# Performance work log

Hardware: AMD Instinct MI355X
Metric: run time of the kernel (lower is better)

Reference implementation:

```python
import jax, jax.numpy as jnp
import numpy as np

L = 2      # layer_num
H = 64     # hid_dim == in_dim (required by final .view(B, N, F))


def setup_inputs() -> dict:
    key = jax.random.key(0)
    k = jax.random.split(key, 5)
    B, T, N, Fd = 64, 48, 256, H
    s = 1.0 / np.sqrt(H)  # PyTorch GRUCell init scale
    return {
        "x": jax.random.normal(k[0], (B, T, N, Fd), dtype=jnp.float32),
        "Wih": jax.random.uniform(k[1], (L, 3 * H, H), minval=-s, maxval=s, dtype=jnp.float32),
        "Whh": jax.random.uniform(k[2], (L, 3 * H, H), minval=-s, maxval=s, dtype=jnp.float32),
        "bih": jax.random.uniform(k[3], (L, 3 * H), minval=-s, maxval=s, dtype=jnp.float32),
        "bhh": jax.random.uniform(k[4], (L, 3 * H), minval=-s, maxval=s, dtype=jnp.float32),
    }


def _ngru_forward(x, Wih, Whh, bih, bhh):
    B, T, N, Fd = x.shape
    # (T, B*N, F): time-major sequence; each layer sees the SAME input x_t
    # (layers are parallel, not stacked, per the original module).
    xs = x.transpose(1, 0, 2, 3).reshape(T, B * N, Fd)
    h0 = jnp.zeros((L, B * N, H), dtype=x.dtype)

    def step(h, x_t):
        # gi: (L, B*N, 3H), gh: (L, B*N, 3H)
        gi = jnp.einsum('bf,lgf->lbg', x_t, Wih) + bih[:, None, :]
        gh = jnp.einsum('lbh,lgh->lbg', h, Whh) + bhh[:, None, :]
        gi_r, gi_z, gi_n = jnp.split(gi, 3, axis=-1)
        gh_r, gh_z, gh_n = jnp.split(gh, 3, axis=-1)
        r = jax.nn.sigmoid(gi_r + gh_r)
        z = jax.nn.sigmoid(gi_z + gh_z)
        n = jnp.tanh(gi_n + r * gh_n)
        h_new = (1.0 - z) * n + z * h
        return h_new, None

    h_final, _ = jax.lax.scan(step, h0, xs)
    # out = h of LAST layer, viewed back as (B, N, F) (requires H == Fd)
    return h_final[-1].reshape(B, N, H)


def reference(x, Wih, Whh, bih, bhh):
    return _ngru_forward(x, Wih, Whh, bih, bhh)
```

## Files before the change

kernel.cpp:

```cpp
#include <hip/hip_runtime.h>
#include <math.h>


#define TT 48
#define HH 64
#define GG 192
#define NN 256
#define RPB 32
#define NTHREADS 256
#define AK 136
#define HBUF (RPB*AK)

typedef _Float16 h8 __attribute__((ext_vector_type(8)));
typedef __attribute__((ext_vector_type(4))) float f32x4;
typedef __attribute__((ext_vector_type(4))) unsigned u32x4;

__device__ __forceinline__ float sigm(float v) {
    return __builtin_amdgcn_rcpf(1.f + __expf(-v));
}
__device__ __forceinline__ float tanh_f(float v) {
    float a = fabsf(v);
    float e = __expf(2.f * a);
    float t = 1.f - 2.f * __builtin_amdgcn_rcpf(e + 1.f);
    return v < 0.f ? -t : t;
}
__device__ __forceinline__ unsigned pkh2(float a, float b) {
    union { _Float16 h[2]; unsigned u; } c;
    c.h[0] = (_Float16)a; c.h[1] = (_Float16)b;
    return c.u;
}

#define MF(A, B, C) __builtin_amdgcn_mfma_f32_16x16x32_f16(A, B, C, 0, 0, 0)

__global__ __launch_bounds__(NTHREADS)
__attribute__((amdgpu_waves_per_eu(2, 2)))
void ngru_mfma11(const float* __restrict__ x,
                 const float* __restrict__ Wih,
                 const float* __restrict__ Whh,
                 const float* __restrict__ bih,
                 const float* __restrict__ bhh,
                 float* __restrict__ out)
{
    extern __shared__ __align__(16) _Float16 lds_h[];

    const int tid  = threadIdx.x;
    const int lane = tid & 63;
    const int nw   = tid >> 6;
    const int c0   = lane & 15;
    const int rq   = lane >> 4;
    const int j    = nw * 16 + c0;
    const bool odd = (c0 & 1);

    const int grow0 = blockIdx.x * RPB;
    const int bb    = grow0 / NN;
    const int n0    = grow0 % NN;

    const float* Wi = Wih + GG * HH;
    const float* Wh = Whh + GG * HH;

    h8 Bf[12];
    #pragma unroll
    for (int g = 0; g < 4; ++g) {
        const int ktlo = (g == 3) ? 2 : 0;
        const int kthi = (g == 2) ? 2 : 4;
        #pragma unroll
        for (int kt = ktlo; kt < kthi; ++kt) {
            const int slot = (g < 2) ? g * 4 + kt : 8 + (g - 2) * 2 + (kt & 1);
            const bool isWi = (kt < 2);
            const int gbase = (g >= 2) ? 2 : g;
            const float* src = (isWi ? Wi : Wh)
                             + (gbase * 64 + j) * HH + (kt & 1) * 32 + rq * 8;
            h8 f;
            #pragma unroll
            for (int q = 0; q < 8; ++q) f[q] = (_Float16)src[q];
            Bf[slot] = f;
        }
    }

    const float brz  = bih[GG + j]      + bhh[GG + j];
    const float bzz  = bih[GG + 64 + j] + bhh[GG + 64 + j];
    const float bin_ = bih[GG + 128 + j];
    const float bhn_ = bhh[GG + 128 + j];
    const f32x4 BIASr = {brz,  brz,  brz,  brz };
    const f32x4 BIASz = {bzz,  bzz,  bzz,  bzz };
    const f32x4 BIASi = {bin_, bin_, bin_, bin_};
    const f32x4 BIASh = {bhn_, bhn_, bhn_, bhn_};

    const int xrow = tid >> 3;
    const int xkc  = (tid & 7) * 8;
    {
        *(u32x4*)(lds_h + xrow * AK + 64 + xkc) = (u32x4){0u, 0u, 0u, 0u};

        const float* xsrc = x + ((size_t)(bb * TT) * NN + n0 + xrow) * HH + xkc;
        float4 p0 = *(const float4*)xsrc;
        float4 p1 = *(const float4*)(xsrc + 4);
        u32x4 w = {pkh2(p0.x, p0.y), pkh2(p0.z, p0.w),
                   pkh2(p1.x, p1.y), pkh2(p1.z, p1.w)};
        *(u32x4*)(lds_h + xrow * AK + xkc) = w;
    }

    float hreg[2][4];
    #pragma unroll
    for (int m = 0; m < 2; ++m)
        #pragma unroll
        for (int r = 0; r < 4; ++r) hreg[m][r] = 0.f;

    __syncthreads();

    for (int t = 0; t < TT; ++t) {
        _Float16* cur = lds_h + (t & 1) * HBUF;
        _Float16* nxt = lds_h + ((t & 1) ^ 1) * HBUF;
        const bool hasNext = (t + 1 < TT);

        float4 p0, p1;
        if (hasNext) {
            const float* xsrc =
                x + ((size_t)(bb * TT + t + 1) * NN + n0 + xrow) * HH + xkc;
            p0 = *(const float4*)xsrc;
            p1 = *(const float4*)(xsrc + 4);
        }

        f32x4 acc[2][4];
        __builtin_amdgcn_s_setprio(1);
        #pragma unroll
        for (int m = 0; m < 2; ++m) {
            const _Float16* ab = cur + (m * 16 + c0) * AK + rq * 8;
            h8 A0 = *(const h8*)(ab);
            h8 A1 = *(const h8*)(ab + 32);
            h8 A2 = *(const h8*)(ab + 64);
            h8 A3 = *(const h8*)(ab + 96);
            f32x4 ar = MF(A0, Bf[0], BIASr);
            ar       = MF(A1, Bf[1], ar);
            ar       = MF(A2, Bf[2], ar);
            ar       = MF(A3, Bf[3], ar);
            f32x4 az = MF(A0, Bf[4], BIASz);
            az       = MF(A1, Bf[5], az);
            az       = MF(A2, Bf[6], az);
            az       = MF(A3, Bf[7], az);
            f32x4 ai = MF(A0, Bf[8], BIASi);
            ai       = MF(A1, Bf[9], ai);
            f32x4 ah = MF(A2, Bf[10], BIASh);
            ah       = MF(A3, Bf[11], ah);
            acc[m][0] = ar; acc[m][1] = az; acc[m][2] = ai; acc[m][3] = ah;
        }
        __builtin_amdgcn_s_setprio(0);

        if (hasNext) {
            u32x4 w = {pkh2(p0.x, p0.y), pkh2(p0.z, p0.w),
                       pkh2(p1.x, p1.y), pkh2(p1.z, p1.w)};
            *(u32x4*)(nxt + xrow * AK + xkc) = w;
        }

        #pragma unroll
        for (int r = 0; r < 4; ++r) {
            float rg0 = sigm(acc[0][0][r]);
            float zg0 = sigm(acc[0][1][r]);
            float ng0 = tanh_f(fmaf(rg0, acc[0][3][r], acc[0][2][r]));
            float hn0 = fmaf(zg0, hreg[0][r] - ng0, ng0);
            hreg[0][r] = hn0;
            float rg1 = sigm(acc[1][0][r]);
            float zg1 = sigm(acc[1][1][r]);
            float ng1 = tanh_f(fmaf(rg1, acc[1][3][r], acc[1][2][r]));
            float hn1 = fmaf(zg1, hreg[1][r] - ng1, ng1);
            hreg[1][r] = hn1;
            if (hasNext) {
                float s0 = __shfl_xor(hn0, 1);
                float s1 = __shfl_xor(hn1, 1);
                unsigned w = odd ? pkh2(s1, hn1) : pkh2(hn0, s0);
                const int row = (odd ? 16 : 0) + rq * 4 + r;
                *(unsigned*)(nxt + row * AK + 64 + (j & ~1)) = w;
            }
        }

        if (hasNext)
            __syncthreads();
    }

    #pragma unroll
    for (int m = 0; m < 2; ++m)
        #pragma unroll
        for (int r = 0; r < 4; ++r)
            out[(size_t)(grow0 + m * 16 + rq * 4 + r) * HH + j] = hreg[m][r];
}

extern "C" void kernel_launch(void* const* d_in, const int* in_sizes, int n_in,
                              void* d_out, int out_size, void* d_ws, size_t ws_size,
                              hipStream_t stream) {
    const float* x   = (const float*)d_in[0];
    const float* Wih = (const float*)d_in[1];
    const float* Whh = (const float*)d_in[2];
    const float* bih = (const float*)d_in[3];
    const float* bhh = (const float*)d_in[4];
    float* out = (float*)d_out;

    const int lds_bytes = 2 * HBUF * (int)sizeof(_Float16);
    (void)hipFuncSetAttribute((const void*)ngru_mfma11,
                        hipFuncAttributeMaxDynamicSharedMemorySize, lds_bytes);

    dim3 grid(16384 / RPB);
    dim3 block(NTHREADS);
    ngru_mfma11<<<grid, block, lds_bytes, stream>>>(x, Wih, Whh, bih, bhh, out);
}
```

Before: 74.14 us.

## Split row tiles across twice as many waves per block

Doubles the block to 512 threads so each wave handles one 16-row M tile instead of two, halving per-wave MFMA and gate work per timestep and shortening the serial recurrence critical path. The hidden-state write drops the shuffle-and-pack in favour of direct per-element fp16 LDS stores, and x staging uses narrower per-thread chunks. In exchange, each block's barrier now spans more waves, the B fragments are duplicated across twice as many waves, and the smaller scalar LDS stores may cost more store instructions.

```diff
diff --git a/kernel.cpp b/kernel.cpp
--- a/kernel.cpp
+++ b/kernel.cpp
@@ -7,13 +7,13 @@
 #define GG 192
 #define NN 256
 #define RPB 32
-#define NTHREADS 256
+#define NTHREADS 512
 #define AK 136
 #define HBUF (RPB*AK)
 
 typedef _Float16 h8 __attribute__((ext_vector_type(8)));
 typedef __attribute__((ext_vector_type(4))) float f32x4;
-typedef __attribute__((ext_vector_type(4))) unsigned u32x4;
+typedef __attribute__((ext_vector_type(2))) unsigned u32x2;
 
 __device__ __forceinline__ float sigm(float v) {
     return __builtin_amdgcn_rcpf(1.f + __expf(-v));
@@ -33,8 +33,8 @@
 #define MF(A, B, C) __builtin_amdgcn_mfma_f32_16x16x32_f16(A, B, C, 0, 0, 0)
 
 __global__ __launch_bounds__(NTHREADS)
-__attribute__((amdgpu_waves_per_eu(2, 2)))
-void ngru_mfma11(const float* __restrict__ x,
+__attribute__((amdgpu_waves_per_eu(4, 4)))
+void ngru_mfma12(const float* __restrict__ x,
                  const float* __restrict__ Wih,
                  const float* __restrict__ Whh,
                  const float* __restrict__ bih,
@@ -45,11 +45,12 @@
 
     const int tid  = threadIdx.x;
     const int lane = tid & 63;
-    const int nw   = tid >> 6;
+    const int wv   = tid >> 6;
+    const int m    = wv >> 2;
+    const int nw   = wv & 3;
     const int c0   = lane & 15;
     const int rq   = lane >> 4;
     const int j    = nw * 16 + c0;
-    const bool odd = (c0 & 1);
 
     const int grow0 = blockIdx.x * RPB;
     const int bb    = grow0 / NN;
@@ -81,29 +82,19 @@
     const float bzz  = bih[GG + 64 + j] + bhh[GG + 64 + j];
     const float bin_ = bih[GG + 128 + j];
     const float bhn_ = bhh[GG + 128 + j];
-    const f32x4 BIASr = {brz,  brz,  brz,  brz };
-    const f32x4 BIASz = {bzz,  bzz,  bzz,  bzz };
-    const f32x4 BIASi = {bin_, bin_, bin_, bin_};
-    const f32x4 BIASh = {bhn_, bhn_, bhn_, bhn_};
 
-    const int xrow = tid >> 3;
-    const int xkc  = (tid & 7) * 8;
+    const int xrow = tid >> 4;
+    const int xc   = (tid & 15) * 4;
     {
-        *(u32x4*)(lds_h + xrow * AK + 64 + xkc) = (u32x4){0u, 0u, 0u, 0u};
-
-        const float* xsrc = x + ((size_t)(bb * TT) * NN + n0 + xrow) * HH + xkc;
-        float4 p0 = *(const float4*)xsrc;
-        float4 p1 = *(const float4*)(xsrc + 4);
-        u32x4 w = {pkh2(p0.x, p0.y), pkh2(p0.z, p0.w),
-                   pkh2(p1.x, p1.y), pkh2(p1.z, p1.w)};
-        *(u32x4*)(lds_h + xrow * AK + xkc) = w;
+        *(u32x2*)(lds_h + xrow * AK + 64 + xc) = (u32x2){0u, 0u};
+        const float* xsrc = x + ((size_t)(bb * TT) * NN + n0 + xrow) * HH + xc;
+        float4 p = *(const float4*)xsrc;
+        *(u32x2*)(lds_h + xrow * AK + xc) = (u32x2){pkh2(p.x, p.y), pkh2(p.z, p.w)};
     }
 
-    float hreg[2][4];
+    float hreg[4];
     #pragma unroll
-    for (int m = 0; m < 2; ++m)
-        #pragma unroll
-        for (int r = 0; r < 4; ++r) hreg[m][r] = 0.f;
+    for (int r = 0; r < 4; ++r) hreg[r] = 0.f;
 
     __syncthreads();
 
@@ -112,75 +103,59 @@
         _Float16* nxt = lds_h + ((t & 1) ^ 1) * HBUF;
         const bool hasNext = (t + 1 < TT);
 
-        float4 p0, p1;
-        if (hasNext) {
-            const float* xsrc =
-                x + ((size_t)(bb * TT + t + 1) * NN + n0 + xrow) * HH + xkc;
-            p0 = *(const float4*)xsrc;
-            p1 = *(const float4*)(xsrc + 4);
-        }
+        float4 p;
+        if (hasNext)
+            p = *(const float4*)(x + ((size_t)(bb * TT + t + 1) * NN
+                                      + n0 + xrow) * HH + xc);
 
-        f32x4 acc[2][4];
+        f32x4 acc0 = {brz,  brz,  brz,  brz };
+        f32x4 acc1 = {bzz,  bzz,  bzz,  bzz };
+        f32x4 acc2 = {bin_, bin_, bin_, bin_};
+        f32x4 acc3 = {bhn_, bhn_, bhn_, bhn_};
+
+        const _Float16* ab = cur + (m * 16 + c0) * AK + rq * 8;
+        h8 A0 = *(const h8*)(ab);
+        h8 A1 = *(const h8*)(ab + 32);
+        h8 A2 = *(const h8*)(ab + 64);
+        h8 A3 = *(const h8*)(ab + 96);
+
         __builtin_amdgcn_s_setprio(1);
-        #pragma unroll
-        for (int m = 0; m < 2; ++m) {
-            const _Float16* ab = cur + (m * 16 + c0) * AK + rq * 8;
-            h8 A0 = *(const h8*)(ab);
-            h8 A1 = *(const h8*)(ab + 32);
-            h8 A2 = *(const h8*)(ab + 64);
-            h8 A3 = *(const h8*)(ab + 96);
-            f32x4 ar = MF(A0, Bf[0], BIASr);
-            ar       = MF(A1, Bf[1], ar);
-            ar       = MF(A2, Bf[2], ar);
-            ar       = MF(A3, Bf[3], ar);
-            f32x4 az = MF(A0, Bf[4], BIASz);
-            az       = MF(A1, Bf[5], az);
-            az       = MF(A2, Bf[6], az);
-            az       = MF(A3, Bf[7], az);
-            f32x4 ai = MF(A0, Bf[8], BIASi);
-            ai       = MF(A1, Bf[9], ai);
-            f32x4 ah = MF(A2, Bf[10], BIASh);
-            ah       = MF(A3, Bf[11], ah);
-            acc[m][0] = ar; acc[m][1] = az; acc[m][2] = ai; acc[m][3] = ah;
-        }
+        acc0 = MF(A0, Bf[0], acc0);
+        acc0 = MF(A1, Bf[1], acc0);
+        acc0 = MF(A2, Bf[2], acc0);
+        acc0 = MF(A3, Bf[3], acc0);
+        acc1 = MF(A0, Bf[4], acc1);
+        acc1 = MF(A1, Bf[5], acc1);
+        acc1 = MF(A2, Bf[6], acc1);
+        acc1 = MF(A3, Bf[7], acc1);
+        acc2 = MF(A0, Bf[8], acc2);
+        acc2 = MF(A1, Bf[9], acc2);
+        acc3 = MF(A2, Bf[10], acc3);
+        acc3 = MF(A3, Bf[11], acc3);
         __builtin_amdgcn_s_setprio(0);
-
-        if (hasNext) {
-            u32x4 w = {pkh2(p0.x, p0.y), pkh2(p0.z, p0.w),
-                       pkh2(p1.x, p1.y), pkh2(p1.z, p1.w)};
-            *(u32x4*)(nxt + xrow * AK + xkc) = w;
-        }
 
         #pragma unroll
         for (int r = 0; r < 4; ++r) {
-            float rg0 = sigm(acc[0][0][r]);
-            float zg0 = sigm(acc[0][1][r]);
-            float ng0 = tanh_f(fmaf(rg0, acc[0][3][r], acc[0][2][r]));
-            float hn0 = fmaf(zg0, hreg[0][r] - ng0, ng0);
-            hreg[0][r] = hn0;
-            float rg1 = sigm(acc[1][0][r]);
-            float zg1 = sigm(acc[1][1][r]);
-            float ng1 = tanh_f(fmaf(rg1, acc[1][3][r], acc[1][2][r]));
-            float hn1 = fmaf(zg1, hreg[1][r] - ng1, ng1);
-            hreg[1][r] = hn1;
-            if (hasNext) {
-                float s0 = __shfl_xor(hn0, 1);
-                float s1 = __shfl_xor(hn1, 1);
-                unsigned w = odd ? pkh2(s1, hn1) : pkh2(hn0, s0);
-                const int row = (odd ? 16 : 0) + rq * 4 + r;
-                *(unsigned*)(nxt + row * AK + 64 + (j & ~1)) = w;
-            }
+            const int row = m * 16 + rq * 4 + r;
+            float rg = sigm(acc0[r]);
+            float zg = sigm(acc1[r]);
+            float ng = tanh_f(fmaf(rg, acc3[r], acc2[r]));
+            float hn = fmaf(zg, hreg[r] - ng, ng);
+            hreg[r] = hn;
+            if (hasNext)
+                nxt[row * AK + 64 + j] = (_Float16)hn;
         }
 
-        if (hasNext)
+        if (hasNext) {
+            *(u32x2*)(nxt + xrow * AK + xc) =
+                (u32x2){pkh2(p.x, p.y), pkh2(p.z, p.w)};
             __syncthreads();
+        }
     }
 
     #pragma unroll
-    for (int m = 0; m < 2; ++m)
-        #pragma unroll
-        for (int r = 0; r < 4; ++r)
-            out[(size_t)(grow0 + m * 16 + rq * 4 + r) * HH + j] = hreg[m][r];
+    for (int r = 0; r < 4; ++r)
+        out[(size_t)(grow0 + m * 16 + rq * 4 + r) * HH + j] = hreg[r];
 }
 
 extern "C" void kernel_launch(void* const* d_in, const int* in_sizes, int n_in,
@@ -194,10 +169,10 @@
     float* out = (float*)d_out;
 
     const int lds_bytes = 2 * HBUF * (int)sizeof(_Float16);
-    (void)hipFuncSetAttribute((const void*)ngru_mfma11,
+    (void)hipFuncSetAttribute((const void*)ngru_mfma12,
                         hipFuncAttributeMaxDynamicSharedMemorySize, lds_bytes);
 
     dim3 grid(16384 / RPB);
     dim3 block(NTHREADS);
-    ngru_mfma11<<<grid, block, lds_bytes, stream>>>(x, Wih, Whh, bih, bhh, out);
+    ngru_mfma12<<<grid, block, lds_bytes, stream>>>(x, Wih, Whh, bih, bhh, out);
 }
```

Result: faster. 68.75 us (-7.3%).
